# Performance work log

Measured on AMD Instinct MI355X. Metric: run time of the kernel, lower is better.

Reference implementation:

```python
import math
import jax, jax.numpy as jnp
from jax import lax
import numpy as np

B, C, H, W = 2, 48, 64, 64
DI, DS, DCONV, DTR = 96, 16, 4, 3   # d_inner=expand*dim, d_state, d_conv, dt_rank=ceil(48/16)
HF = 96                              # SEFN hidden = dim * ffn_expansion_factor(2)


def _posenc(L, d):
    pos = jnp.arange(L, dtype=jnp.float32)[:, None]
    div = jnp.exp(jnp.arange(0, d, 2, dtype=jnp.float32) * (-math.log(10000.0) / d))
    pe = jnp.zeros((L, d), jnp.float32)
    pe = pe.at[:, 0::2].set(jnp.sin(pos * div))
    pe = pe.at[:, 1::2].set(jnp.cos(pos * div))
    return pe


def _ln(x, w, b, eps=1e-5):  # last-dim LayerNorm, biased variance (torch unbiased=False)
    mu = x.mean(-1, keepdims=True)
    var = ((x - mu) ** 2).mean(-1, keepdims=True)
    return (x - mu) / jnp.sqrt(var + eps) * w + b


def _ln4d(x, w, b):  # WithBias LayerNorm over channel dim of NCHW (to_3d/to_4d round trip)
    b_, c_, h_, w_ = x.shape
    xf = x.reshape(b_, c_, h_ * w_).transpose(0, 2, 1)
    return _ln(xf, w, b).transpose(0, 2, 1).reshape(b_, c_, h_, w_)


def _flip_odd(x):  # flip last axis on odd rows of axis -2 (snake reordering)
    return x.at[:, :, 1::2, :].set(x[:, :, 1::2, ::-1])


def _conv2d(x, w, bias=None, groups=1, pad=0):
    y = lax.conv_general_dilated(x, w, (1, 1), [(pad, pad), (pad, pad)],
                                 feature_group_count=groups,
                                 dimension_numbers=('NCHW', 'OIHW', 'NCHW'))
    if bias is not None:
        y = y + bias[None, :, None, None]
    return y


def _mamba(x, inproj, convw, convb, xproj, dtw, dtb, Alog, D, outproj):
    # standard mamba_ssm Mamba forward; x: (B, L, C)
    b_, L, _ = x.shape
    xz = x @ inproj.T                      # (B, L, 2*DI)
    xm, z = xz[..., :DI], xz[..., DI:]
    xc = xm.transpose(0, 2, 1)             # (B, DI, L)
    xc = lax.conv_general_dilated(xc, convw, (1,), [(DCONV - 1, 0)],
                                  feature_group_count=DI,
                                  dimension_numbers=('NCH', 'OIH', 'NCH'))
    xc = jax.nn.silu(xc + convb[None, :, None]).transpose(0, 2, 1)  # (B, L, DI)
    x_dbl = xc @ xproj.T                   # (B, L, DTR + 2*DS)
    dt = jax.nn.softplus(x_dbl[..., :DTR] @ dtw.T + dtb)            # (B, L, DI)
    Bm = x_dbl[..., DTR:DTR + DS]          # (B, L, DS)
    Cm = x_dbl[..., DTR + DS:]             # (B, L, DS)
    A = -jnp.exp(Alog)                     # (DI, DS)
    dA = jnp.exp(dt[..., None] * A)        # (B, L, DI, DS)
    dBx = dt[..., None] * Bm[:, :, None, :] * xc[..., None]

    def step(h, t):
        dA_t, dBx_t, C_t = t
        h = dA_t * h + dBx_t
        return h, jnp.einsum('bds,bs->bd', h, C_t)

    h0 = jnp.zeros((b_, DI, DS), x.dtype)
    _, ys = lax.scan(step, h0, (dA.transpose(1, 0, 2, 3), dBx.transpose(1, 0, 2, 3), Cm.transpose(1, 0, 2)))
    y = ys.transpose(1, 0, 2) + xc * D
    y = y * jax.nn.silu(z)
    return y @ outproj.T


def _forward(x, n1_w, n1_b, n2_w, n2_b, mln1_w, mln1_b, mln2_w, mln2_b,
             m1, m2, f_pin, f_dw, f_fus, f_dwa, f_pout,
             f_c1w, f_c1b, f_ln1_w, f_ln1_b, f_c2w, f_c2b, f_ln2_w, f_ln2_b):
    x_spatial = x
    L = H * W
    pe = _posenc(L, C)
    # --- MambaLayer: bidirectional flip-scan ---
    xn = _ln4d(x, n1_w, n1_b)
    rev1 = _flip_odd(xn)                               # snake order over rows
    rev2 = _flip_odd(xn.transpose(0, 1, 3, 2))         # snake order over cols
    x1_flat = rev1.reshape(B, C, L).transpose(0, 2, 1) + pe
    x2_flat = rev2.reshape(B, C, L).transpose(0, 2, 1) + pe
    y1 = _mamba(_ln(x1_flat, mln1_w, mln1_b), *m1)
    y2 = _mamba(_ln(x2_flat, mln2_w, mln2_b), *m2)
    out1 = _flip_odd(y1.transpose(0, 2, 1).reshape(B, C, H, W))
    out2 = _flip_odd(y2.transpose(0, 2, 1).reshape(B, C, W, H)).transpose(0, 1, 3, 2)
    x = x + out1 + out2
    # --- SEFN ---
    xn2 = _ln4d(x, n2_w, n2_b)
    xp = _conv2d(xn2, f_pin)                           # (B, 2*HF, H, W)
    y = x_spatial.reshape(B, C, H // 2, 2, W // 2, 2).mean((3, 5))   # AvgPool2d(2)
    y = jax.nn.relu(_ln4d(_conv2d(y, f_c1w, f_c1b, pad=1), f_ln1_w, f_ln1_b))
    y = jax.nn.relu(_ln4d(_conv2d(y, f_c2w, f_c2b, pad=1), f_ln2_w, f_ln2_b))
    y = jnp.repeat(jnp.repeat(y, 2, axis=2), 2, axis=3)              # nearest Upsample(2)
    xd = _conv2d(xp, f_dw, groups=2 * HF, pad=1)
    x1, x2 = xd[:, :HF], xd[:, HF:]
    x1 = _conv2d(jnp.concatenate([x1, y], axis=1), f_fus)
    x1 = _conv2d(x1, f_dwa, groups=HF, pad=1)
    ff = _conv2d(jax.nn.gelu(x1, approximate=False) * x2, f_pout)
    return x + ff


def setup_inputs():
    key = jax.random.key(0)
    ks = iter(jax.random.split(key, 64))

    def nrm(shape, s):
        return s * jax.random.normal(next(ks), shape, jnp.float32)

    inp = {}
    inp['x'] = nrm((B, C, H, W), 1.0)
    for nm in ['n1', 'n2', 'mln1', 'mln2', 'f_ln1', 'f_ln2']:
        inp[nm + '_w'] = jnp.ones((C,), jnp.float32)
        inp[nm + '_b'] = jnp.zeros((C,), jnp.float32)
    for p in ['m1', 'm2']:
        inp[p + '_inproj'] = nrm((2 * DI, C), 0.1)
        inp[p + '_convw'] = nrm((DI, 1, DCONV), 0.3)
        inp[p + '_convb'] = jnp.zeros((DI,), jnp.float32)
        inp[p + '_xproj'] = nrm((DTR + 2 * DS, DI), 0.1)
        inp[p + '_dtw'] = nrm((DI, DTR), 0.3)
        u = jax.random.uniform(next(ks), (DI,), jnp.float32)
        inp[p + '_dtb'] = jnp.log(jnp.expm1(0.001 + 0.099 * u))  # mamba dt bias init
        inp[p + '_Alog'] = jnp.log(jnp.tile(jnp.arange(1., DS + 1., dtype=jnp.float32), (DI, 1)))
        inp[p + '_D'] = jnp.ones((DI,), jnp.float32)
        inp[p + '_outproj'] = nrm((C, DI), 0.1)
    inp['f_pin'] = nrm((2 * HF, C, 1, 1), 0.1)
    inp['f_dw'] = nrm((2 * HF, 1, 3, 3), 0.2)
    inp['f_fus'] = nrm((HF, HF + C, 1, 1), 0.08)
    inp['f_dwa'] = nrm((HF, 1, 3, 3), 0.2)
    inp['f_pout'] = nrm((C, HF, 1, 1), 0.1)
    inp['f_c1w'] = nrm((C, C, 3, 3), 0.05)
    inp['f_c1b'] = jnp.zeros((C,), jnp.float32)
    inp['f_c2w'] = nrm((C, C, 3, 3), 0.05)
    inp['f_c2b'] = jnp.zeros((C,), jnp.float32)
    return inp


def reference(x, n1_w, n1_b, n2_w, n2_b, mln1_w, mln1_b, mln2_w, mln2_b,
              m1_inproj, m1_convw, m1_convb, m1_xproj, m1_dtw, m1_dtb, m1_Alog, m1_D, m1_outproj,
              m2_inproj, m2_convw, m2_convb, m2_xproj, m2_dtw, m2_dtb, m2_Alog, m2_D, m2_outproj,
              f_pin, f_dw, f_fus, f_dwa, f_pout,
              f_c1w, f_c1b, f_ln1_w, f_ln1_b, f_c2w, f_c2b, f_ln2_w, f_ln2_b):
    m1 = (m1_inproj, m1_convw, m1_convb, m1_xproj, m1_dtw, m1_dtb, m1_Alog, m1_D, m1_outproj)
    m2 = (m2_inproj, m2_convw, m2_convb, m2_xproj, m2_dtw, m2_dtb, m2_Alog, m2_D, m2_outproj)
    return _forward(x, n1_w, n1_b, n2_w, n2_b, mln1_w, mln1_b, mln2_w, mln2_b,
                    m1, m2, f_pin, f_dw, f_fus, f_dwa, f_pout,
                    f_c1w, f_c1b, f_ln1_w, f_ln1_b, f_c2w, f_c2b, f_ln2_w, f_ln2_b)
```

## Files before the change

kernel.cpp:

```cpp
#include <hip/hip_runtime.h>

#define DEV __device__ __forceinline__

DEV float siluf(float x){ return x / (1.f + __expf(-x)); }
DEV float softplusf(float x){ return fmaxf(x, 0.f) + log1pf(expf(-fabsf(x))); }
DEV float geluf(float x){ return 0.5f * x * (1.f + erff(x * 0.70710678118654752440f)); }

__global__ __launch_bounds__(256) void kA_front(const float* __restrict__ x,
    const float* __restrict__ n1w, const float* __restrict__ n1b,
    const float* __restrict__ mw0, const float* __restrict__ mb0,
    const float* __restrict__ mw1, const float* __restrict__ mb1,
    const float* __restrict__ ip0, const float* __restrict__ ip1,
    float* __restrict__ xmg, float* __restrict__ Vg){
  __shared__ alignas(16) float Vl[48*36];
  __shared__ float Wt[48*97];
  __shared__ float mu_s[32], rs_s[32];
  int bd = blockIdx.x >> 7, tile = blockIdx.x & 127;
  int dir = bd >> 1, b = bd & 1;
  int t0 = tile*32;
  int tid = threadIdx.x;
  const float* ip = dir ? ip1 : ip0;
  const float* mw = dir ? mw1 : mw0;
  const float* mb = dir ? mb1 : mb0;
  for (int i = tid; i < 96*48; i += 256){
    int j = i / 48, c = i % 48;
    Wt[c*97 + j] = ip[i];
  }
  for (int i = tid; i < 48*32; i += 256){
    int c = i >> 5, r = i & 31;
    int t = t0 + r;
    int h, w;
    if (dir == 0){ h = t >> 6; int wp = t & 63; w = (h & 1) ? 63 - wp : wp; }
    else         { w = t >> 6; int hp = t & 63; h = (w & 1) ? 63 - hp : hp; }
    Vl[c*36 + r] = x[(size_t)b*48*4096 + c*4096 + h*64 + w];
  }
  __syncthreads();
  {
    int r = tid >> 3, k = tid & 7;
    float s1 = 0.f, s2 = 0.f;
    #pragma unroll
    for (int cc = 0; cc < 6; cc++){
      float v = Vl[(k*6+cc)*36 + r];
      s1 += v; s2 += v*v;
    }
    s1 += __shfl_xor(s1,1); s2 += __shfl_xor(s2,1);
    s1 += __shfl_xor(s1,2); s2 += __shfl_xor(s2,2);
    s1 += __shfl_xor(s1,4); s2 += __shfl_xor(s2,4);
    if (k == 0){
      float m = s1*(1.f/48.f);
      mu_s[r] = m;
      rs_s[r] = rsqrtf(s2*(1.f/48.f) - m*m + 1e-5f);
    }
  }
  __syncthreads();
  for (int i = tid; i < 32*48; i += 256){
    int r = i / 48, c = i % 48;
    int t = t0 + r;
    float v = Vl[c*36 + r];
    float xn = (v - mu_s[r])*rs_s[r]*n1w[c] + n1b[c];
    float ang = (float)t * __expf(-(float)(c & ~1) * (9.210340371976184f/48.f));
    float pe = (c & 1) ? cosf(ang) : sinf(ang);
    Vl[c*36 + r] = xn + pe;
  }
  __syncthreads();
  {
    int r = tid >> 3, k = tid & 7;
    float s1 = 0.f, s2 = 0.f;
    #pragma unroll
    for (int cc = 0; cc < 6; cc++){
      float v = Vl[(k*6+cc)*36 + r];
      s1 += v; s2 += v*v;
    }
    s1 += __shfl_xor(s1,1); s2 += __shfl_xor(s2,1);
    s1 += __shfl_xor(s1,2); s2 += __shfl_xor(s2,2);
    s1 += __shfl_xor(s1,4); s2 += __shfl_xor(s2,4);
    if (k == 0){
      float m = s1*(1.f/48.f);
      mu_s[r] = m;
      rs_s[r] = rsqrtf(s2*(1.f/48.f) - m*m + 1e-5f);
    }
  }
  __syncthreads();
  for (int i = tid; i < 32*48; i += 256){
    int r = i / 48, c = i % 48;
    float v = Vl[c*36 + r];
    float v2 = (v - mu_s[r])*rs_s[r]*mw[c] + mb[c];
    Vl[c*36 + r] = v2;
    Vg[((size_t)bd*4096 + t0 + r)*48 + c] = v2;
  }
  __syncthreads();
  for (int k = 0; k < 3; k++){
    int i = tid + k*256;
    int j = i % 96, rb = i / 96;
    float a0=0.f, a1=0.f, a2=0.f, a3=0.f;
    #pragma unroll 4
    for (int c = 0; c < 48; c++){
      float wv = Wt[c*97 + j];
      const float4 v4 = *(const float4*)&Vl[c*36 + rb*4];
      a0 += wv*v4.x; a1 += wv*v4.y; a2 += wv*v4.z; a3 += wv*v4.w;
    }
    size_t g = ((size_t)bd*4096 + t0 + rb*4)*96 + j;
    xmg[g] = a0; xmg[g+96] = a1; xmg[g+192] = a2; xmg[g+288] = a3;
  }
}

__global__ __launch_bounds__(384) void kB_convscan(const float* __restrict__ xmg,
    const float* __restrict__ cwp0, const float* __restrict__ cwp1,
    const float* __restrict__ cbp0, const float* __restrict__ cbp1,
    const float* __restrict__ xpp0, const float* __restrict__ xpp1,
    const float* __restrict__ dwp0, const float* __restrict__ dwp1,
    const float* __restrict__ dbp0, const float* __restrict__ dbp1,
    const float* __restrict__ Alog0, const float* __restrict__ Alog1,
    float* __restrict__ xcg, float* __restrict__ dtg,
    float* __restrict__ Bmg, float* __restrict__ Cmg,
    float* __restrict__ P, float* __restrict__ S){
  __shared__ union UB {
    float xml[96*36];
    struct { float xwl[35*96]; float xdbl[35*33]; } p;
  } ub;
  __shared__ float xcl[96*33];
  __shared__ float dtl[96*33];
  __shared__ alignas(16) float Bl[32*16], Cl[32*16];
  __shared__ float cw[96*4], cbv[96], dwl[96*3], dbl[96];
  int bd = blockIdx.x >> 7, tile = blockIdx.x & 127;
  int dir = bd >> 1;
  int t0 = tile*32;
  int tid = threadIdx.x;
  const float* cwp = dir ? cwp1 : cwp0;
  const float* cbp = dir ? cbp1 : cbp0;
  const float* xpp = dir ? xpp1 : xpp0;
  const float* dwp = dir ? dwp1 : dwp0;
  const float* dbp = dir ? dbp1 : dbp0;
  const float* Alog = dir ? Alog1 : Alog0;
  for (int i = tid; i < 35*96; i += 384){
    int tl = i / 96, d = i % 96;
    int t = t0 - 3 + tl;
    ub.xml[d*36 + tl] = (t >= 0) ? xmg[((size_t)bd*4096 + t)*96 + d] : 0.f;
  }
  for (int i = tid; i < 96*4;  i += 384) cw[i] = cwp[i];
  for (int i = tid; i < 96*3;  i += 384) dwl[i] = dwp[i];
  for (int i = tid; i < 96;    i += 384){ cbv[i] = cbp[i]; dbl[i] = dbp[i]; }
  __syncthreads();
  for (int i = tid; i < 96*32; i += 384){
    int d = i >> 5, t = i & 31;
    float acc = cbv[d];
    #pragma unroll
    for (int k = 0; k < 4; k++) acc += cw[d*4+k]*ub.xml[d*36 + t + k];
    xcl[d*33 + t] = siluf(acc);
  }
  __syncthreads();
  for (int i = tid; i < 35*96; i += 384) ub.p.xwl[i] = xpp[i];
  __syncthreads();
  for (int i = tid; i < 35*32; i += 384){
    int j = i / 32, t = i % 32;
    float acc = 0.f;
    #pragma unroll 4
    for (int d = 0; d < 96; d++) acc += xcl[d*33 + t]*ub.p.xwl[j*96 + d];
    ub.p.xdbl[j*33 + t] = acc;
  }
  __syncthreads();
  for (int i = tid; i < 96*32; i += 384){
    int d = i >> 5, t = i & 31;
    float v = dbl[d];
    #pragma unroll
    for (int r = 0; r < 3; r++) v += ub.p.xdbl[r*33 + t]*dwl[d*3 + r];
    dtl[d*33 + t] = softplusf(v);
  }
  for (int i = tid; i < 32*16; i += 384){
    int t = i / 16, s = i % 16;
    Bl[t*16 + s] = ub.p.xdbl[(3+s)*33 + t];
    Cl[t*16 + s] = ub.p.xdbl[(19+s)*33 + t];
  }
  __syncthreads();
  for (int i = tid; i < 32*96; i += 384){
    int t = i / 96, d = i % 96;
    size_t g = ((size_t)bd*4096 + t0 + t)*96 + d;
    xcg[g] = xcl[d*33 + t];
    dtg[g] = dtl[d*33 + t];
  }
  for (int i = tid; i < 32*16; i += 384){
    int t = i / 16, s = i % 16;
    size_t g = ((size_t)bd*4096 + t0 + t)*16 + s;
    Bmg[g] = Bl[t*16 + s];
    Cmg[g] = Cl[t*16 + s];
  }
  {
    int d = tid >> 2, q = tid & 3;
    float A0 = -__expf(Alog[d*16 + q*4 + 0]);
    float A1 = -__expf(Alog[d*16 + q*4 + 1]);
    float A2 = -__expf(Alog[d*16 + q*4 + 2]);
    float A3 = -__expf(Alog[d*16 + q*4 + 3]);
    float h0=0.f,h1=0.f,h2=0.f,h3=0.f, p0=1.f,p1=1.f,p2=1.f,p3=1.f;
    #pragma unroll 4
    for (int t = 0; t < 32; t++){
      float dtd = dtl[d*33 + t];
      float u = dtd * xcl[d*33 + t];
      const float4 b4 = *(const float4*)&Bl[t*16 + q*4];
      float a0 = __expf(dtd*A0), a1 = __expf(dtd*A1), a2 = __expf(dtd*A2), a3 = __expf(dtd*A3);
      h0 = a0*h0 + u*b4.x; p0 *= a0;
      h1 = a1*h1 + u*b4.y; p1 *= a1;
      h2 = a2*h2 + u*b4.z; p2 *= a2;
      h3 = a3*h3 + u*b4.w; p3 *= a3;
    }
    size_t ob = (size_t)blockIdx.x*1536 + d*16 + q*4;
    *(float4*)&P[ob] = make_float4(p0,p1,p2,p3);
    *(float4*)&S[ob] = make_float4(h0,h1,h2,h3);
  }
}

__global__ __launch_bounds__(256) void k4_comb(float* __restrict__ P, const float* __restrict__ S){
  int tid2 = blockIdx.x*256 + threadIdx.x;
  int bd = tid2 / 1536, r = tid2 % 1536;
  size_t idx = (size_t)bd*128*1536 + r;
  const int ST = 1536;
  float pb0,pb1,pb2,pb3,pb4,pb5,pb6,pb7, sb0,sb1,sb2,sb3,sb4,sb5,sb6,sb7;
  pb0=P[idx+0*ST]; sb0=S[idx+0*ST]; pb1=P[idx+1*ST]; sb1=S[idx+1*ST];
  pb2=P[idx+2*ST]; sb2=S[idx+2*ST]; pb3=P[idx+3*ST]; sb3=S[idx+3*ST];
  pb4=P[idx+4*ST]; sb4=S[idx+4*ST]; pb5=P[idx+5*ST]; sb5=S[idx+5*ST];
  pb6=P[idx+6*ST]; sb6=S[idx+6*ST]; pb7=P[idx+7*ST]; sb7=S[idx+7*ST];
  float h = 0.f;
  for (int c0 = 0; c0 < 128; c0 += 8){
    float pn0=0,sn0=0,pn1=0,sn1=0,pn2=0,sn2=0,pn3=0,sn3=0;
    float pn4=0,sn4=0,pn5=0,sn5=0,pn6=0,sn6=0,pn7=0,sn7=0;
    if (c0 + 8 < 128){
      pn0=P[idx+(size_t)(c0+8)*ST];  sn0=S[idx+(size_t)(c0+8)*ST];
      pn1=P[idx+(size_t)(c0+9)*ST];  sn1=S[idx+(size_t)(c0+9)*ST];
      pn2=P[idx+(size_t)(c0+10)*ST]; sn2=S[idx+(size_t)(c0+10)*ST];
      pn3=P[idx+(size_t)(c0+11)*ST]; sn3=S[idx+(size_t)(c0+11)*ST];
      pn4=P[idx+(size_t)(c0+12)*ST]; sn4=S[idx+(size_t)(c0+12)*ST];
      pn5=P[idx+(size_t)(c0+13)*ST]; sn5=S[idx+(size_t)(c0+13)*ST];
      pn6=P[idx+(size_t)(c0+14)*ST]; sn6=S[idx+(size_t)(c0+14)*ST];
      pn7=P[idx+(size_t)(c0+15)*ST]; sn7=S[idx+(size_t)(c0+15)*ST];
    }
    P[idx+(size_t)(c0+0)*ST] = h; h = pb0*h + sb0;
    P[idx+(size_t)(c0+1)*ST] = h; h = pb1*h + sb1;
    P[idx+(size_t)(c0+2)*ST] = h; h = pb2*h + sb2;
    P[idx+(size_t)(c0+3)*ST] = h; h = pb3*h + sb3;
    P[idx+(size_t)(c0+4)*ST] = h; h = pb4*h + sb4;
    P[idx+(size_t)(c0+5)*ST] = h; h = pb5*h + sb5;
    P[idx+(size_t)(c0+6)*ST] = h; h = pb6*h + sb6;
    P[idx+(size_t)(c0+7)*ST] = h; h = pb7*h + sb7;
    pb0=pn0;sb0=sn0;pb1=pn1;sb1=sn1;pb2=pn2;sb2=sn2;pb3=pn3;sb3=sn3;
    pb4=pn4;sb4=sn4;pb5=pn5;sb5=sn5;pb6=pn6;sb6=sn6;pb7=pn7;sb7=sn7;
  }
}

__global__ __launch_bounds__(384) void k5_scan2(const float* __restrict__ dtg,
    const float* __restrict__ xcg, const float* __restrict__ Bmg, const float* __restrict__ Cmg,
    const float* __restrict__ Alog0, const float* __restrict__ Alog1,
    const float* __restrict__ Dp0, const float* __restrict__ Dp1,
    const float* __restrict__ ip0, const float* __restrict__ ip1,
    const float* __restrict__ Vg, const float* __restrict__ Hin, float* __restrict__ yout){
  __shared__ union U5 {
    struct { float dts[32*96]; float xcs[32*96]; } s;
    struct { float Wzt[48*96]; float Vgs[32*48]; } e;
  } u;
  __shared__ alignas(16) float Bl[32*16], Cl[32*16];
  __shared__ float yl[32*96];
  int task = blockIdx.x;
  int bd = task >> 7, ch = task & 127;
  int t0 = ch*32;
  int tid = threadIdx.x;
  const float* ip   = (bd >= 2) ? ip1 : ip0;
  const float* Alog = (bd >= 2) ? Alog1 : Alog0;
  const float* Dp   = (bd >= 2) ? Dp1 : Dp0;
  for (int i = tid; i < 32*96; i += 384){
    int t = i / 96, dd = i % 96;
    size_t g = ((size_t)bd*4096 + t0 + t)*96 + dd;
    u.s.dts[i] = dtg[g];
    u.s.xcs[i] = xcg[g];
  }
  for (int i = tid; i < 32*16; i += 384){
    size_t g = ((size_t)bd*4096 + t0)*16 + i;
    Bl[i] = Bmg[g];
    Cl[i] = Cmg[g];
  }
  __syncthreads();
  {
    int d = tid >> 2, q = tid & 3;
    float A0 = -__expf(Alog[d*16 + q*4 + 0]);
    float A1 = -__expf(Alog[d*16 + q*4 + 1]);
    float A2 = -__expf(Alog[d*16 + q*4 + 2]);
    float A3 = -__expf(Alog[d*16 + q*4 + 3]);
    float Dd = Dp[d];
    const float4 h4 = *(const float4*)&Hin[(size_t)task*1536 + d*16 + q*4];
    float h0 = h4.x, h1 = h4.y, h2 = h4.z, h3 = h4.w;
    for (int t = 0; t < 32; t += 2){
      float dtdA = u.s.dts[t*96 + d];
      float xcvA = u.s.xcs[t*96 + d];
      float dtdB = u.s.dts[(t+1)*96 + d];
      float xcvB = u.s.xcs[(t+1)*96 + d];
      float uA = dtdA * xcvA, uB = dtdB * xcvB;
      const float4 b4A = *(const float4*)&Bl[t*16 + q*4];
      const float4 c4A = *(const float4*)&Cl[t*16 + q*4];
      const float4 b4B = *(const float4*)&Bl[(t+1)*16 + q*4];
      const float4 c4B = *(const float4*)&Cl[(t+1)*16 + q*4];
      float a0 = __expf(dtdA*A0), a1 = __expf(dtdA*A1), a2 = __expf(dtdA*A2), a3 = __expf(dtdA*A3);
      float e0 = __expf(dtdB*A0), e1 = __expf(dtdB*A1), e2 = __expf(dtdB*A2), e3 = __expf(dtdB*A3);
      h0 = a0*h0 + uA*b4A.x;
      h1 = a1*h1 + uA*b4A.y;
      h2 = a2*h2 + uA*b4A.z;
      h3 = a3*h3 + uA*b4A.w;
      float pyA = (h0*c4A.x + h1*c4A.y) + (h2*c4A.z + h3*c4A.w);
      h0 = e0*h0 + uB*b4B.x;
      h1 = e1*h1 + uB*b4B.y;
      h2 = e2*h2 + uB*b4B.z;
      h3 = e3*h3 + uB*b4B.w;
      float pyB = (h0*c4B.x + h1*c4B.y) + (h2*c4B.z + h3*c4B.w);
      pyA += __shfl_xor(pyA, 1);  pyB += __shfl_xor(pyB, 1);
      pyA += __shfl_xor(pyA, 2);  pyB += __shfl_xor(pyB, 2);
      if (q == 0){
        yl[t*96 + d]     = pyA + xcvA*Dd;
        yl[(t+1)*96 + d] = pyB + xcvB*Dd;
      }
    }
  }
  __syncthreads();
  for (int i = tid; i < 96*48; i += 384){
    int j = i % 96, c = i / 96;
    u.e.Wzt[c*96 + j] = ip[(96 + j)*48 + c];
  }
  for (int i = tid; i < 32*48; i += 384){
    int t = i / 48, c = i % 48;
    u.e.Vgs[i] = Vg[((size_t)bd*4096 + t0 + t)*48 + c];
  }
  __syncthreads();
  for (int i = tid; i < 32*96; i += 384){
    int t = i / 96, dd = i % 96;
    float z = 0.f;
    #pragma unroll 4
    for (int c = 0; c < 48; c++) z += u.e.Wzt[c*96 + dd] * u.e.Vgs[t*48 + c];
    size_t g = ((size_t)bd*4096 + t0 + t)*96 + dd;
    yout[g] = yl[i] * siluf(z);
  }
}

__global__ __launch_bounds__(384) void k67_mid(const float* __restrict__ x,
    const float* __restrict__ y1, const float* __restrict__ y2,
    const float* __restrict__ op1, const float* __restrict__ op2,
    const float* __restrict__ nw, const float* __restrict__ nb,
    const float* __restrict__ pin,
    float* __restrict__ xmid, float* __restrict__ xp){
  __shared__ float bufW[192*48];
  __shared__ union UL { float ylds[32*97]; struct { float xl[48*33]; float mu[32]; float rs[32]; } l; } ul;
  int bid = blockIdx.x;
  int b = bid >> 7, h = (bid >> 1) & 63, wh = bid & 1;
  int w0 = wh << 5;
  int tid = threadIdx.x;
  int w = tid & 31, cq = tid >> 5;
  float acc[4] = {0,0,0,0};
  for (int pass = 0; pass < 2; pass++){
    __syncthreads();
    const float* op = pass ? op2 : op1;
    const float* y  = pass ? y2  : y1;
    for (int i = tid; i < 48*96; i += 384) bufW[i] = op[i];
    if (pass == 0){
      for (int i = tid; i < 32*96; i += 384){
        int wl_ = i / 96, d = i % 96;
        int wsp = w0 + wl_;
        int wp = (h & 1) ? 63 - wsp : wsp;
        ul.ylds[wl_*97 + d] = y[((size_t)b*4096 + h*64 + wp)*96 + d];
      }
    } else {
      for (int i = tid; i < 32*96; i += 384){
        int wl_ = i / 96, d = i % 96;
        int wsp = w0 + wl_;
        int t = wsp*64 + ((wsp & 1) ? 63 - h : h);
        ul.ylds[wl_*97 + d] = y[((size_t)b*4096 + t)*96 + d];
      }
    }
    __syncthreads();
    #pragma unroll 4
    for (int d = 0; d < 96; d++){
      float yv = ul.ylds[w*97 + d];
      acc[0] += yv * bufW[(cq*4+0)*96 + d];
      acc[1] += yv * bufW[(cq*4+1)*96 + d];
      acc[2] += yv * bufW[(cq*4+2)*96 + d];
      acc[3] += yv * bufW[(cq*4+3)*96 + d];
    }
  }
  __syncthreads();
  #pragma unroll
  for (int q = 0; q < 4; q++){
    int c = cq*4 + q;
    size_t idx = (((size_t)b*48 + c)*64 + h)*64 + w0 + w;
    float v = x[idx] + acc[q];
    xmid[idx] = v;
    ul.l.xl[c*33 + w] = v;
  }
  for (int i = tid; i < 192*48; i += 384) bufW[i] = pin[i];
  __syncthreads();
  if (tid < 256){
    int r = tid >> 3, k = tid & 7;
    float s1 = 0.f, s2 = 0.f;
    #pragma unroll
    for (int cc = 0; cc < 6; cc++){
      float v = ul.l.xl[(k*6+cc)*33 + r];
      s1 += v; s2 += v*v;
    }
    s1 += __shfl_xor(s1,1); s2 += __shfl_xor(s2,1);
    s1 += __shfl_xor(s1,2); s2 += __shfl_xor(s2,2);
    s1 += __shfl_xor(s1,4); s2 += __shfl_xor(s2,4);
    if (k == 0){
      float m = s1*(1.f/48.f);
      ul.l.mu[r] = m;
      ul.l.rs[r] = rsqrtf(s2*(1.f/48.f) - m*m + 1e-5f);
    }
  }
  __syncthreads();
  for (int i = tid; i < 48*32; i += 384){
    int c = i >> 5, ww = i & 31;
    ul.l.xl[c*33 + ww] = (ul.l.xl[c*33 + ww] - ul.l.mu[ww])*ul.l.rs[ww]*nw[c] + nb[c];
  }
  __syncthreads();
  for (int it = 0; it < 4; it++){
    int i = tid + it*384;
    int ww = i & 31, oq = i >> 5; int o0 = oq*4;
    float a0=0,a1=0,a2=0,a3=0;
    #pragma unroll 4
    for (int c = 0; c < 48; c++){
      float xv = ul.l.xl[c*33 + ww];
      a0 += xv*bufW[(o0+0)*48+c];
      a1 += xv*bufW[(o0+1)*48+c];
      a2 += xv*bufW[(o0+2)*48+c];
      a3 += xv*bufW[(o0+3)*48+c];
    }
    xp[(((size_t)b*192 + o0+0)*64 + h)*64 + w0 + ww] = a0;
    xp[(((size_t)b*192 + o0+1)*64 + h)*64 + w0 + ww] = a1;
    xp[(((size_t)b*192 + o0+2)*64 + h)*64 + w0 + ww] = a2;
    xp[(((size_t)b*192 + o0+3)*64 + h)*64 + w0 + ww] = a3;
  }
}

__global__ __launch_bounds__(384) void k9_conv3(const float* __restrict__ in,
    const float* __restrict__ wgt, const float* __restrict__ bias,
    const float* __restrict__ lnw, const float* __restrict__ lnb,
    float* __restrict__ out, int pooled, int lnin){
  __shared__ float wl[12*48*9];
  __shared__ float sin_[48*3*34];
  __shared__ float mu_i[104], rs_i[104];
  int bid = blockIdx.x;
  int cq = bid & 3, i0 = (bid >> 2) & 31, b = bid >> 7;
  int tid = threadIdx.x;
  for (int i = tid; i < 12*48*9; i += 384) wl[i] = wgt[cq*12*48*9 + i];
  for (int i = tid; i < 48*3*34; i += 384){
    int jx = i % 34, ky = (i/34) % 3, ci = i/102;
    int r = i0 + ky - 1, j = jx - 1;
    float v = 0.f;
    if (r >= 0 && r < 32 && j >= 0 && j < 32){
      if (pooled){
        const float* xb = in + (((size_t)b*48 + ci)*64 + 2*r)*64 + 2*j;
        v = 0.25f*(xb[0] + xb[1] + xb[64] + xb[65]);
      } else {
        v = in[(((size_t)b*48 + ci)*32 + r)*32 + j];
      }
    }
    sin_[i] = v;
  }
  __syncthreads();
  if (lnin){
    if (tid < 102){
      int jx = tid % 34, ky = tid / 34;
      int r = i0 + ky - 1, j = jx - 1;
      if (r >= 0 && r < 32 && j >= 0 && j < 32){
        float s1 = 0.f, s2 = 0.f;
        #pragma unroll 4
        for (int ci = 0; ci < 48; ci++){ float v = sin_[ci*102 + tid]; s1 += v; s2 += v*v; }
        float m = s1*(1.f/48.f);
        mu_i[tid] = m;
        rs_i[tid] = rsqrtf(s2*(1.f/48.f) - m*m + 1e-5f);
      }
    }
    __syncthreads();
    for (int i = tid; i < 48*102; i += 384){
      int ci = i / 102, p = i % 102;
      int jx = p % 34, ky = p / 34;
      int r = i0 + ky - 1, j = jx - 1;
      if (r >= 0 && r < 32 && j >= 0 && j < 32){
        float v = (sin_[i] - mu_i[p])*rs_i[p]*lnw[ci] + lnb[ci];
        sin_[i] = fmaxf(v, 0.f);
      }
    }
    __syncthreads();
  }
  int j = tid & 31, col = tid >> 5;
  float acc = bias[cq*12 + col];
  for (int ci = 0; ci < 48; ci++){
    const float* wp = wl + ((size_t)col*48 + ci)*9;
    const float* sp = sin_ + ci*102;
    #pragma unroll
    for (int ky = 0; ky < 3; ky++)
      #pragma unroll
      for (int kx = 0; kx < 3; kx++)
        acc += sp[ky*34 + j + kx] * wp[ky*3 + kx];
  }
  out[(((size_t)b*48 + cq*12 + col)*32 + i0)*32 + j] = acc;
}

__global__ __launch_bounds__(256) void k13_dw(const float* __restrict__ in,
    const float* __restrict__ wgt, float* __restrict__ out, int CH){
  int idx = blockIdx.x*256 + threadIdx.x;
  if (idx >= 2*CH*1024) return;
  int wq = idx & 15, h = (idx >> 4) & 63, c = (idx >> 10) % CH, b = idx / (CH*1024);
  int w0 = wq*4;
  const float* ip = in + ((size_t)b*CH + c)*4096;
  const float* wp = wgt + c*9;
  float a0=0.f,a1=0.f,a2=0.f,a3=0.f;
  #pragma unroll
  for (int ky = 0; ky < 3; ky++){
    int hh = h + ky - 1;
    if (hh < 0 || hh > 63) continue;
    const float* rp = ip + hh*64;
    float v0 = (w0 > 0)  ? rp[w0-1] : 0.f;
    float v1 = rp[w0+0], v2 = rp[w0+1], v3 = rp[w0+2], v4 = rp[w0+3];
    float v5 = (w0 < 60) ? rp[w0+4] : 0.f;
    float k0 = wp[ky*3+0], k1 = wp[ky*3+1], k2 = wp[ky*3+2];
    a0 += k0*v0 + k1*v1 + k2*v2;
    a1 += k0*v1 + k1*v2 + k2*v3;
    a2 += k0*v2 + k1*v3 + k2*v4;
    a3 += k0*v3 + k1*v4 + k2*v5;
  }
  float* op = out + (((size_t)b*CH + c)*64 + h)*64 + w0;
  op[0]=a0; op[1]=a1; op[2]=a2; op[3]=a3;
}

__global__ __launch_bounds__(256) void k14_fus(const float* __restrict__ xd,
    const float* __restrict__ cv2, const float* __restrict__ lnw, const float* __restrict__ lnb,
    const float* __restrict__ fus, float* __restrict__ x1){
  __shared__ float wl[48*144];
  __shared__ float al[96][64];
  __shared__ float yl[48][32];
  __shared__ float muy[32], rsy[32];
  int bid = blockIdx.x;
  int oh = bid & 1, h = (bid >> 1) & 63, b = bid >> 7;
  int tid = threadIdx.x;
  for (int i = tid; i < 48*144; i += 256) wl[i] = fus[(size_t)oh*48*144 + i];
  for (int i = tid; i < 96*64; i += 256){
    int ci = i >> 6, w = i & 63;
    al[ci][w] = xd[(((size_t)b*192 + ci)*64 + h)*64 + w];
  }
  for (int i = tid; i < 48*32; i += 256){
    int cj = i >> 5, j = i & 31;
    yl[cj][j] = cv2[(((size_t)b*48 + cj)*32 + (h >> 1))*32 + j];
  }
  __syncthreads();
  if (tid < 32){
    float s1 = 0.f, s2 = 0.f;
    #pragma unroll 4
    for (int cj = 0; cj < 48; cj++){ float v = yl[cj][tid]; s1 += v; s2 += v*v; }
    float m = s1*(1.f/48.f);
    muy[tid] = m;
    rsy[tid] = rsqrtf(s2*(1.f/48.f) - m*m + 1e-5f);
  }
  __syncthreads();
  for (int i = tid; i < 48*32; i += 256){
    int cj = i >> 5, j = i & 31;
    yl[cj][j] = fmaxf((yl[cj][j] - muy[j])*rsy[j]*lnw[cj] + lnb[cj], 0.f);
  }
  __syncthreads();
  for (int it = 0; it < 3; it++){
    int i = tid + it*256;
    int w = i & 63, ob = i >> 6; int o0 = ob*4;
    float a[4] = {0,0,0,0};
    #pragma unroll 4
    for (int ci = 0; ci < 96; ci++){
      float xv = al[ci][w];
      #pragma unroll
      for (int q = 0; q < 4; q++) a[q] += xv * wl[(o0+q)*144 + ci];
    }
    int w2 = w >> 1;
    #pragma unroll 4
    for (int cj = 0; cj < 48; cj++){
      float yv = yl[cj][w2];
      #pragma unroll
      for (int q = 0; q < 4; q++) a[q] += yv * wl[(o0+q)*144 + 96 + cj];
    }
    #pragma unroll
    for (int q = 0; q < 4; q++)
      x1[(((size_t)b*96 + oh*48 + o0 + q)*64 + h)*64 + w] = a[q];
  }
}

__global__ __launch_bounds__(384) void k16_out(const float* __restrict__ x1,
    const float* __restrict__ xd, const float* __restrict__ dww,
    const float* __restrict__ pout, const float* __restrict__ xmid, float* __restrict__ out){
  __shared__ float wl[48*96];
  __shared__ float xs[96*3*34];
  __shared__ float gl[96*33];
  __shared__ float dwl[96*9];
  int bid = blockIdx.x;
  int b = bid >> 7, h = (bid >> 1) & 63, wh = bid & 1;
  int w0 = wh << 5;
  int tid = threadIdx.x;
  for (int i = tid; i < 48*96; i += 384) wl[i] = pout[i];
  for (int i = tid; i < 96*9; i += 384) dwl[i] = dww[i];
  for (int i = tid; i < 96*3*34; i += 384){
    int jx = i % 34, ky = (i/34) % 3, ch = i/102;
    int hh = h + ky - 1, ww_ = w0 + jx - 1;
    float v = 0.f;
    if (hh >= 0 && hh < 64 && ww_ >= 0 && ww_ < 64)
      v = x1[(((size_t)b*96 + ch)*64 + hh)*64 + ww_];
    xs[i] = v;
  }
  __syncthreads();
  for (int i = tid; i < 96*32; i += 384){
    int ch = i >> 5, ww = i & 31;
    const float* wp = dwl + ch*9;
    const float* sp = xs + ch*102;
    float a = 0.f;
    #pragma unroll
    for (int ky = 0; ky < 3; ky++)
      #pragma unroll
      for (int kx = 0; kx < 3; kx++)
        a += sp[ky*34 + ww + kx] * wp[ky*3 + kx];
    float x2 = xd[(((size_t)b*192 + 96 + ch)*64 + h)*64 + w0 + ww];
    gl[ch*33 + ww] = geluf(a) * x2;
  }
  __syncthreads();
  int ww = tid & 31, cq = tid >> 5;
  float a0=0,a1=0,a2=0,a3=0;
  #pragma unroll 4
  for (int ch = 0; ch < 96; ch++){
    float gv = gl[ch*33 + ww];
    a0 += gv * wl[(cq*4+0)*96 + ch];
    a1 += gv * wl[(cq*4+1)*96 + ch];
    a2 += gv * wl[(cq*4+2)*96 + ch];
    a3 += gv * wl[(cq*4+3)*96 + ch];
  }
  #pragma unroll
  for (int q = 0; q < 4; q++){
    int c = cq*4 + q;
    size_t idx = (((size_t)b*48 + c)*64 + h)*64 + w0 + ww;
    float av = (q==0)?a0:(q==1)?a1:(q==2)?a2:a3;
    out[idx] = xmid[idx] + av;
  }
}

extern "C" void kernel_launch(void* const* d_in, const int* in_sizes, int n_in,
                              void* d_out, int out_size, void* d_ws, size_t ws_size,
                              hipStream_t stream){
  (void)in_sizes; (void)n_in; (void)out_size; (void)ws_size;
  const float* x    = (const float*)d_in[0];
  const float* n1w  = (const float*)d_in[1];
  const float* n1b  = (const float*)d_in[2];
  const float* n2w  = (const float*)d_in[3];
  const float* n2b  = (const float*)d_in[4];
  const float* mlnw[2] = {(const float*)d_in[5], (const float*)d_in[7]};
  const float* mlnb[2] = {(const float*)d_in[6], (const float*)d_in[8]};
  const float* fln1w = (const float*)d_in[9];
  const float* fln1b = (const float*)d_in[10];
  const float* fln2w = (const float*)d_in[11];
  const float* fln2b = (const float*)d_in[12];
  const float* inproj[2]  = {(const float*)d_in[13], (const float*)d_in[22]};
  const float* convw[2]   = {(const float*)d_in[14], (const float*)d_in[23]};
  const float* convb[2]   = {(const float*)d_in[15], (const float*)d_in[24]};
  const float* xproj[2]   = {(const float*)d_in[16], (const float*)d_in[25]};
  const float* dtw[2]     = {(const float*)d_in[17], (const float*)d_in[26]};
  const float* dtbp[2]    = {(const float*)d_in[18], (const float*)d_in[27]};
  const float* Alog[2]    = {(const float*)d_in[19], (const float*)d_in[28]};
  const float* Dp[2]      = {(const float*)d_in[20], (const float*)d_in[29]};
  const float* outproj[2] = {(const float*)d_in[21], (const float*)d_in[30]};
  const float* fpin  = (const float*)d_in[31];
  const float* fdw   = (const float*)d_in[32];
  const float* ffus  = (const float*)d_in[33];
  const float* fdwa  = (const float*)d_in[34];
  const float* fpout = (const float*)d_in[35];
  const float* fc1w  = (const float*)d_in[36];
  const float* fc1b  = (const float*)d_in[37];
  const float* fc2w  = (const float*)d_in[38];
  const float* fc2b  = (const float*)d_in[39];

  float* ws = (float*)d_ws;
  float* xmg = ws + 0;
  float* Vgb = ws + 1572864;
  float* xcg = ws + 2359296;
  float* dtg = ws + 3932160;
  float* Bmg = ws + 5505024;
  float* Cmg = ws + 5767168;
  float* Pb  = ws + 6029312;
  float* Sb  = ws + 6815744;
  float* xmid= ws + 7602176;
  float* yall = xmg;
  float* Hin  = Pb;
  float* ta   = Sb;
  float* tbuf = Sb + 98304;
  float* xpb  = xcg;
  float* xdb  = dtg;
  float* x1b  = Pb;

  kA_front<<<512,256,0,stream>>>(x, n1w, n1b,
      mlnw[0], mlnb[0], mlnw[1], mlnb[1], inproj[0], inproj[1], xmg, Vgb);
  kB_convscan<<<512,384,0,stream>>>(xmg,
      convw[0], convw[1], convb[0], convb[1], xproj[0], xproj[1],
      dtw[0], dtw[1], dtbp[0], dtbp[1], Alog[0], Alog[1],
      xcg, dtg, Bmg, Cmg, Pb, Sb);
  k4_comb  <<<24,256,0,stream>>>(Pb, Sb);
  k5_scan2 <<<512,384,0,stream>>>(dtg, xcg, Bmg, Cmg, Alog[0], Alog[1],
      Dp[0], Dp[1], inproj[0], inproj[1], Vgb, Hin, yall);
  k67_mid  <<<256,384,0,stream>>>(x, yall, yall + 786432, outproj[0], outproj[1],
      n2w, n2b, fpin, xmid, xpb);
  k9_conv3 <<<256,384,0,stream>>>(x,  fc1w, fc1b, fln1w, fln1b, ta,   1, 0);
  k9_conv3 <<<256,384,0,stream>>>(ta, fc2w, fc2b, fln1w, fln1b, tbuf, 0, 1);
  k13_dw   <<<1536,256,0,stream>>>(xpb, fdw, xdb, 192);
  k14_fus  <<<256,256,0,stream>>>(xdb, tbuf, fln2w, fln2b, ffus, x1b);
  k16_out  <<<256,384,0,stream>>>(x1b, xdb, fdwa, fpout, xmid, (float*)d_out);
}
```

Baseline: 190.3 us.

## Fuse front LayerNorm/in-projection kernel into conv-scan kernel with halo recompute

```diff
diff --git a/kernel.cpp b/kernel.cpp
--- a/kernel.cpp
+++ b/kernel.cpp
@@ -6,146 +6,152 @@
 DEV float softplusf(float x){ return fmaxf(x, 0.f) + log1pf(expf(-fabsf(x))); }
 DEV float geluf(float x){ return 0.5f * x * (1.f + erff(x * 0.70710678118654752440f)); }
 
-__global__ __launch_bounds__(256) void kA_front(const float* __restrict__ x,
+__global__ __launch_bounds__(384) void kAB(const float* __restrict__ x,
     const float* __restrict__ n1w, const float* __restrict__ n1b,
     const float* __restrict__ mw0, const float* __restrict__ mb0,
     const float* __restrict__ mw1, const float* __restrict__ mb1,
     const float* __restrict__ ip0, const float* __restrict__ ip1,
-    float* __restrict__ xmg, float* __restrict__ Vg){
-  __shared__ alignas(16) float Vl[48*36];
-  __shared__ float Wt[48*97];
-  __shared__ float mu_s[32], rs_s[32];
-  int bd = blockIdx.x >> 7, tile = blockIdx.x & 127;
-  int dir = bd >> 1, b = bd & 1;
-  int t0 = tile*32;
-  int tid = threadIdx.x;
-  const float* ip = dir ? ip1 : ip0;
-  const float* mw = dir ? mw1 : mw0;
-  const float* mb = dir ? mb1 : mb0;
-  for (int i = tid; i < 96*48; i += 256){
-    int j = i / 48, c = i % 48;
-    Wt[c*97 + j] = ip[i];
-  }
-  for (int i = tid; i < 48*32; i += 256){
-    int c = i >> 5, r = i & 31;
-    int t = t0 + r;
-    int h, w;
-    if (dir == 0){ h = t >> 6; int wp = t & 63; w = (h & 1) ? 63 - wp : wp; }
-    else         { w = t >> 6; int hp = t & 63; h = (w & 1) ? 63 - hp : hp; }
-    Vl[c*36 + r] = x[(size_t)b*48*4096 + c*4096 + h*64 + w];
-  }
-  __syncthreads();
-  {
-    int r = tid >> 3, k = tid & 7;
-    float s1 = 0.f, s2 = 0.f;
-    #pragma unroll
-    for (int cc = 0; cc < 6; cc++){
-      float v = Vl[(k*6+cc)*36 + r];
-      s1 += v; s2 += v*v;
-    }
-    s1 += __shfl_xor(s1,1); s2 += __shfl_xor(s2,1);
-    s1 += __shfl_xor(s1,2); s2 += __shfl_xor(s2,2);
-    s1 += __shfl_xor(s1,4); s2 += __shfl_xor(s2,4);
-    if (k == 0){
-      float m = s1*(1.f/48.f);
-      mu_s[r] = m;
-      rs_s[r] = rsqrtf(s2*(1.f/48.f) - m*m + 1e-5f);
-    }
-  }
-  __syncthreads();
-  for (int i = tid; i < 32*48; i += 256){
-    int r = i / 48, c = i % 48;
-    int t = t0 + r;
-    float v = Vl[c*36 + r];
-    float xn = (v - mu_s[r])*rs_s[r]*n1w[c] + n1b[c];
-    float ang = (float)t * __expf(-(float)(c & ~1) * (9.210340371976184f/48.f));
-    float pe = (c & 1) ? cosf(ang) : sinf(ang);
-    Vl[c*36 + r] = xn + pe;
-  }
-  __syncthreads();
-  {
-    int r = tid >> 3, k = tid & 7;
-    float s1 = 0.f, s2 = 0.f;
-    #pragma unroll
-    for (int cc = 0; cc < 6; cc++){
-      float v = Vl[(k*6+cc)*36 + r];
-      s1 += v; s2 += v*v;
-    }
-    s1 += __shfl_xor(s1,1); s2 += __shfl_xor(s2,1);
-    s1 += __shfl_xor(s1,2); s2 += __shfl_xor(s2,2);
-    s1 += __shfl_xor(s1,4); s2 += __shfl_xor(s2,4);
-    if (k == 0){
-      float m = s1*(1.f/48.f);
-      mu_s[r] = m;
-      rs_s[r] = rsqrtf(s2*(1.f/48.f) - m*m + 1e-5f);
-    }
-  }
-  __syncthreads();
-  for (int i = tid; i < 32*48; i += 256){
-    int r = i / 48, c = i % 48;
-    float v = Vl[c*36 + r];
-    float v2 = (v - mu_s[r])*rs_s[r]*mw[c] + mb[c];
-    Vl[c*36 + r] = v2;
-    Vg[((size_t)bd*4096 + t0 + r)*48 + c] = v2;
-  }
-  __syncthreads();
-  for (int k = 0; k < 3; k++){
-    int i = tid + k*256;
-    int j = i % 96, rb = i / 96;
-    float a0=0.f, a1=0.f, a2=0.f, a3=0.f;
-    #pragma unroll 4
-    for (int c = 0; c < 48; c++){
-      float wv = Wt[c*97 + j];
-      const float4 v4 = *(const float4*)&Vl[c*36 + rb*4];
-      a0 += wv*v4.x; a1 += wv*v4.y; a2 += wv*v4.z; a3 += wv*v4.w;
-    }
-    size_t g = ((size_t)bd*4096 + t0 + rb*4)*96 + j;
-    xmg[g] = a0; xmg[g+96] = a1; xmg[g+192] = a2; xmg[g+288] = a3;
-  }
-}
-
-__global__ __launch_bounds__(384) void kB_convscan(const float* __restrict__ xmg,
     const float* __restrict__ cwp0, const float* __restrict__ cwp1,
     const float* __restrict__ cbp0, const float* __restrict__ cbp1,
     const float* __restrict__ xpp0, const float* __restrict__ xpp1,
     const float* __restrict__ dwp0, const float* __restrict__ dwp1,
     const float* __restrict__ dbp0, const float* __restrict__ dbp1,
     const float* __restrict__ Alog0, const float* __restrict__ Alog1,
-    float* __restrict__ xcg, float* __restrict__ dtg,
+    float* __restrict__ Vg, float* __restrict__ xcg, float* __restrict__ dtg,
     float* __restrict__ Bmg, float* __restrict__ Cmg,
     float* __restrict__ P, float* __restrict__ S){
   __shared__ union UB {
-    float xml[96*36];
+    float Wt[48*98];
     struct { float xwl[35*96]; float xdbl[35*33]; } p;
   } ub;
+  __shared__ alignas(16) float Vl[48*36];
+  __shared__ float xml[96*36];
   __shared__ float xcl[96*33];
   __shared__ float dtl[96*33];
   __shared__ alignas(16) float Bl[32*16], Cl[32*16];
   __shared__ float cw[96*4], cbv[96], dwl[96*3], dbl[96];
+  __shared__ float mu_s[40], rs_s[40];
   int bd = blockIdx.x >> 7, tile = blockIdx.x & 127;
-  int dir = bd >> 1;
+  int dir = bd >> 1, b = bd & 1;
   int t0 = tile*32;
   int tid = threadIdx.x;
+  const float* ip  = dir ? ip1  : ip0;
+  const float* mw  = dir ? mw1  : mw0;
+  const float* mb  = dir ? mb1  : mb0;
   const float* cwp = dir ? cwp1 : cwp0;
   const float* cbp = dir ? cbp1 : cbp0;
   const float* xpp = dir ? xpp1 : xpp0;
   const float* dwp = dir ? dwp1 : dwp0;
   const float* dbp = dir ? dbp1 : dbp0;
   const float* Alog = dir ? Alog1 : Alog0;
-  for (int i = tid; i < 35*96; i += 384){
-    int tl = i / 96, d = i % 96;
-    int t = t0 - 3 + tl;
-    ub.xml[d*36 + tl] = (t >= 0) ? xmg[((size_t)bd*4096 + t)*96 + d] : 0.f;
+  for (int i = tid; i < 96*48; i += 384){
+    int j = i / 48, c = i % 48;
+    ub.Wt[c*98 + j] = ip[i];
+  }
+  for (int i = tid; i < 48*35; i += 384){
+    int c = i / 35, iv = i % 35;
+    int t = (iv < 32) ? (t0 + iv) : (t0 - 35 + iv);
+    float v = 0.f;
+    if (t >= 0){
+      int h, w;
+      if (dir == 0){ h = t >> 6; int wp = t & 63; w = (h & 1) ? 63 - wp : wp; }
+      else         { w = t >> 6; int hp = t & 63; h = (w & 1) ? 63 - hp : hp; }
+      v = x[(size_t)b*48*4096 + c*4096 + h*64 + w];
+    }
+    Vl[c*36 + iv] = v;
   }
   for (int i = tid; i < 96*4;  i += 384) cw[i] = cwp[i];
   for (int i = tid; i < 96*3;  i += 384) dwl[i] = dwp[i];
   for (int i = tid; i < 96;    i += 384){ cbv[i] = cbp[i]; dbl[i] = dbp[i]; }
+  __syncthreads();
+  {
+    int r = tid >> 3, k = tid & 7;
+    if (r < 35){
+      float s1 = 0.f, s2 = 0.f;
+      #pragma unroll
+      for (int cc = 0; cc < 6; cc++){
+        float v = Vl[(k*6+cc)*36 + r];
+        s1 += v; s2 += v*v;
+      }
+      s1 += __shfl_xor(s1,1); s2 += __shfl_xor(s2,1);
+      s1 += __shfl_xor(s1,2); s2 += __shfl_xor(s2,2);
+      s1 += __shfl_xor(s1,4); s2 += __shfl_xor(s2,4);
+      if (k == 0){
+        float m = s1*(1.f/48.f);
+        mu_s[r] = m;
+        rs_s[r] = rsqrtf(s2*(1.f/48.f) - m*m + 1e-5f);
+      }
+    }
+  }
+  __syncthreads();
+  for (int i = tid; i < 35*48; i += 384){
+    int iv = i / 48, c = i % 48;
+    int t = (iv < 32) ? (t0 + iv) : (t0 - 35 + iv);
+    if (t >= 0){
+      float v = Vl[c*36 + iv];
+      float xn = (v - mu_s[iv])*rs_s[iv]*n1w[c] + n1b[c];
+      float ang = (float)t * __expf(-(float)(c & ~1) * (9.210340371976184f/48.f));
+      float pe = (c & 1) ? cosf(ang) : sinf(ang);
+      Vl[c*36 + iv] = xn + pe;
+    }
+  }
+  __syncthreads();
+  {
+    int r = tid >> 3, k = tid & 7;
+    if (r < 35){
+      float s1 = 0.f, s2 = 0.f;
+      #pragma unroll
+      for (int cc = 0; cc < 6; cc++){
+        float v = Vl[(k*6+cc)*36 + r];
+        s1 += v; s2 += v*v;
+      }
+      s1 += __shfl_xor(s1,1); s2 += __shfl_xor(s2,1);
+      s1 += __shfl_xor(s1,2); s2 += __shfl_xor(s2,2);
+      s1 += __shfl_xor(s1,4); s2 += __shfl_xor(s2,4);
+      if (k == 0){
+        float m = s1*(1.f/48.f);
+        mu_s[r] = m;
+        rs_s[r] = rsqrtf(s2*(1.f/48.f) - m*m + 1e-5f);
+      }
+    }
+  }
+  __syncthreads();
+  for (int i = tid; i < 35*48; i += 384){
+    int iv = i / 48, c = i % 48;
+    int t = (iv < 32) ? (t0 + iv) : (t0 - 35 + iv);
+    float v2 = 0.f;
+    if (t >= 0) v2 = (Vl[c*36 + iv] - mu_s[iv])*rs_s[iv]*mw[c] + mb[c];
+    Vl[c*36 + iv] = v2;
+    if (iv < 32) Vg[((size_t)bd*4096 + t0 + iv)*48 + c] = v2;
+  }
+  __syncthreads();
+  for (int it = 0; it < 2; it++){
+    int i = tid + it*384;
+    int j = i % 96, rb = i / 96;
+    float a0=0.f, a1=0.f, a2=0.f, a3=0.f;
+    #pragma unroll 4
+    for (int c = 0; c < 48; c++){
+      float wv = ub.Wt[c*98 + j];
+      const float4 v4 = *(const float4*)&Vl[c*36 + rb*4];
+      a0 += wv*v4.x; a1 += wv*v4.y; a2 += wv*v4.z; a3 += wv*v4.w;
+    }
+    int tl = rb*4 + 3;
+    xml[j*36 + tl+0] = a0; xml[j*36 + tl+1] = a1;
+    xml[j*36 + tl+2] = a2; xml[j*36 + tl+3] = a3;
+  }
+  for (int i = tid; i < 96*3; i += 384){
+    int j = i % 96, rh = i / 96;
+    float a = 0.f;
+    #pragma unroll 4
+    for (int c = 0; c < 48; c++) a += ub.Wt[c*98 + j] * Vl[c*36 + 32 + rh];
+    xml[j*36 + rh] = a;
+  }
   __syncthreads();
   for (int i = tid; i < 96*32; i += 384){
     int d = i >> 5, t = i & 31;
     float acc = cbv[d];
     #pragma unroll
-    for (int k = 0; k < 4; k++) acc += cw[d*4+k]*ub.xml[d*36 + t + k];
+    for (int k = 0; k < 4; k++) acc += cw[d*4+k]*xml[d*36 + t + k];
     xcl[d*33 + t] = siluf(acc);
   }
   __syncthreads();
@@ -671,7 +677,7 @@
   const float* fc2b  = (const float*)d_in[39];
 
   float* ws = (float*)d_ws;
-  float* xmg = ws + 0;
+  float* yall= ws + 0;
   float* Vgb = ws + 1572864;
   float* xcg = ws + 2359296;
   float* dtg = ws + 3932160;
@@ -680,7 +686,6 @@
   float* Pb  = ws + 6029312;
   float* Sb  = ws + 6815744;
   float* xmid= ws + 7602176;
-  float* yall = xmg;
   float* Hin  = Pb;
   float* ta   = Sb;
   float* tbuf = Sb + 98304;
@@ -688,12 +693,11 @@
   float* xdb  = dtg;
   float* x1b  = Pb;
 
-  kA_front<<<512,256,0,stream>>>(x, n1w, n1b,
-      mlnw[0], mlnb[0], mlnw[1], mlnb[1], inproj[0], inproj[1], xmg, Vgb);
-  kB_convscan<<<512,384,0,stream>>>(xmg,
+  kAB<<<512,384,0,stream>>>(x, n1w, n1b,
+      mlnw[0], mlnb[0], mlnw[1], mlnb[1], inproj[0], inproj[1],
       convw[0], convw[1], convb[0], convb[1], xproj[0], xproj[1],
       dtw[0], dtw[1], dtbp[0], dtbp[1], Alog[0], Alog[1],
-      xcg, dtg, Bmg, Cmg, Pb, Sb);
+      Vgb, xcg, dtg, Bmg, Cmg, Pb, Sb);
   k4_comb  <<<24,256,0,stream>>>(Pb, Sb);
   k5_scan2 <<<512,384,0,stream>>>(dtg, xcg, Bmg, Cmg, Alog[0], Alog[1],
       Dp[0], Dp[1], inproj[0], inproj[1], Vgb, Hin, yall);
```

After: 204.0 us. +7.2%, slower.
